# Performance work log

Measured on AMD Instinct MI355X. Metric: run time of the kernel, lower is better.

## Reference

```python
import jax, jax.numpy as jnp
import numpy as np

N_TOKENS = 32768
D_MODEL = 1024


def setup_inputs() -> dict:
    key = jax.random.key(0)
    kx, kr, kw1, kb1, kw2, kb2 = jax.random.split(key, 6)
    scale = 1.0 / np.sqrt(D_MODEL)
    x = jax.random.normal(kx, (N_TOKENS, D_MODEL), dtype=jnp.float32)
    # RandomScatterRouter: each token independently routed to one of 2 experts
    route = jax.random.randint(kr, (N_TOKENS,), 0, 2, dtype=jnp.int32)
    W1 = jax.random.normal(kw1, (D_MODEL, D_MODEL), dtype=jnp.float32) * scale
    b1 = jax.random.normal(kb1, (D_MODEL,), dtype=jnp.float32) * scale
    W2 = jax.random.normal(kw2, (D_MODEL, D_MODEL), dtype=jnp.float32) * scale
    b2 = jax.random.normal(kb2, (D_MODEL,), dtype=jnp.float32) * scale
    return {"x": x, "W1": W1, "b1": b1, "W2": W2, "b2": b2, "route": route}


def reference(x, W1, b1, W2, b2, route):
    # Semantics of scatter -> expert linears -> gather(reverse_indice):
    #   out[i] = x[i] @ W_{route[i]} + b_{route[i]}  (original token order restored)
    # jit-friendly form: mask-partition tokens to each expert (m0 + m1 == 1),
    # run the two expert GEMMs on the disjoint partitions, sum to recombine.
    m0 = (route == 0).astype(x.dtype)[:, None]  # [N, 1]
    m1 = 1.0 - m0
    y0 = (x * m0) @ W1 + b1 * m0  # expert-1 output on its tokens, zeros elsewhere
    y1 = (x * m1) @ W2 + b2 * m1  # expert-2 output on its tokens, zeros elsewhere
    return y0 + y1
```

## Files before the change

### kernel.cpp

```cpp
#include <hip/hip_runtime.h>

#define NT 32768
#define DM 1024
#define NTOT (NT + 128)
#define NKT (DM / 64)

typedef __bf16 bf16x8 __attribute__((ext_vector_type(8)));
typedef float f32x4 __attribute__((ext_vector_type(4)));

#define GLD16(g, l)                                                            \
  __builtin_amdgcn_global_load_lds(                                            \
      (const __attribute__((address_space(1))) void*)(g),                      \
      (__attribute__((address_space(3))) void*)(l), 16, 0, 0)

__device__ __forceinline__ unsigned short f2bf(float f) {
  unsigned u = __float_as_uint(f);
  u += 0x7fffu + ((u >> 16) & 1u);
  return (unsigned short)(u >> 16);
}

__global__ void wt_k(const float* __restrict__ W1, const float* __restrict__ W2,
                     unsigned short* __restrict__ Wt) {
  const float* __restrict__ W = blockIdx.z ? W2 : W1;
  unsigned short* __restrict__ dst = Wt + (size_t)blockIdx.z * DM * DM;
  __shared__ float tile[32][33];
  int tx = threadIdx.x, ty = threadIdx.y;
  int n0 = blockIdx.x * 32, k0 = blockIdx.y * 32;
#pragma unroll
  for (int i = 0; i < 32; i += 8)
    tile[ty + i][tx] = W[(size_t)(k0 + ty + i) * DM + n0 + tx];
  __syncthreads();
#pragma unroll
  for (int i = 0; i < 32; i += 8)
    dst[(size_t)(n0 + ty + i) * DM + k0 + tx] = f2bf(tile[tx][ty + i]);
}

__global__ __launch_bounds__(64) void route_k(const int* __restrict__ route,
                                              int* __restrict__ idx,
                                              int* __restrict__ counters) {
  const int lane = threadIdx.x;
  const int token = blockIdx.x * 64 + lane;
  int r = route[token];
  unsigned long long m0 = __ballot(r == 0);
  unsigned long long lt = (1ULL << lane) - 1ULL;
  int rank0 = __popcll(m0 & lt);
  int rank1 = lane - rank0;
  int cnt0 = __popcll(m0);
  int base0 = 0, base1 = 0;
  if (lane == 0) {
    base0 = atomicAdd(&counters[0], cnt0);
    base1 = atomicAdd(&counters[1], 64 - cnt0);
  }
  base0 = __shfl(base0, 0, 64);
  base1 = __shfl(base1, 0, 64);
  int slot = (r == 0) ? (base0 + rank0) : (NTOT - 1 - (base1 + rank1));
  idx[slot] = token;
}

__global__ __launch_bounds__(256, 3) void gemm_k(
    const float* __restrict__ x,
    const unsigned short* __restrict__ Wt,
    const float* __restrict__ b1, const float* __restrict__ b2,
    const int* __restrict__ idx, const int* __restrict__ counters,
    float* __restrict__ out) {
  __shared__ unsigned short As[128 * 64];
  __shared__ unsigned short Bs[2][128 * 64];

  const int t = threadIdx.x;
  const int lane = t & 63, wave = t >> 6;

  const int lin = blockIdx.y * 8 + blockIdx.x;
  const int L = (lin & 7) * 257 + (lin >> 3);
  const int row0 = (L >> 3) * 128;
  const int col0 = (L & 7) * 128;

  const int n0 = counters[0];
  const int expert = (row0 < n0) ? 0 : 1;
  const unsigned short* Wte = Wt + (size_t)expert * DM * DM;
  const float* bias = expert ? b2 : b1;

  const int wr = (wave >> 1) * 64;
  const int wc = (wave & 1) * 64;
  const int lr = lane & 15;

  const int rsub = t >> 4;
  const int c16 = t & 15;
  const float* rowp[8];
#pragma unroll
  for (int p = 0; p < 8; ++p) {
    int gr = row0 + p * 16 + rsub;
    int tok = idx[gr];
    if (gr >= n0 && gr < n0 + 128) tok = 0;
    rowp[p] = x + (size_t)tok * DM;
  }

  float4 a[8];
  f32x4 acc[4][4] = {};

#define LOADA(k0)                                                              \
  _Pragma("unroll") for (int p = 0; p < 8; ++p)                                \
      a[p] = *(const float4*)(rowp[p] + (k0) + c16 * 4);

#define WRITEA()                                                               \
  _Pragma("unroll") for (int p = 0; p < 8; ++p) {                              \
    int r = p * 16 + rsub;                                                     \
    int off = (r * 8 + ((c16 >> 1) ^ (r & 7))) * 16 + (c16 & 1) * 8;           \
    union { unsigned short h[4]; ushort4 u4; } pk;                             \
    pk.h[0] = f2bf(a[p].x); pk.h[1] = f2bf(a[p].y);                            \
    pk.h[2] = f2bf(a[p].z); pk.h[3] = f2bf(a[p].w);                            \
    *(ushort4*)((char*)&As[0] + off) = pk.u4;                                  \
  }

#define STAGEB(k0, bufw)                                                       \
  _Pragma("unroll") for (int p = 0; p < 4; ++p) {                              \
    int q = p * 256 + t;                                                       \
    int r = q >> 3;                                                            \
    int c = ((q & 7) ^ (r & 7)) * 8;                                           \
    GLD16(Wte + (size_t)(col0 + r) * DM + (k0) + c, &Bs[bufw][q * 8]);         \
  }

  LOADA(0);
  STAGEB(0, 0);

  for (int kt = 0; kt < NKT; ++kt) {
    const int buf = kt & 1;
    WRITEA();
    __syncthreads();
    if (kt < NKT - 1) {
      LOADA((kt + 1) * 64);
      STAGEB((kt + 1) * 64, buf ^ 1);
    }
#pragma unroll
    for (int s = 0; s < 2; ++s) {
      const int cb = s * 4 + (lane >> 4);
      bf16x8 af[4], bfr[4];
#pragma unroll
      for (int i = 0; i < 4; ++i) {
        int r = wr + i * 16 + lr;
        af[i] = *(const bf16x8*)&As[(r * 8 + (cb ^ (r & 7))) * 8];
      }
#pragma unroll
      for (int j = 0; j < 4; ++j) {
        int r = wc + j * 16 + lr;
        bfr[j] = *(const bf16x8*)&Bs[buf][(r * 8 + (cb ^ (r & 7))) * 8];
      }
#pragma unroll
      for (int i = 0; i < 4; ++i)
#pragma unroll
        for (int j = 0; j < 4; ++j)
          acc[i][j] = __builtin_amdgcn_mfma_f32_16x16x32_bf16(af[i], bfr[j], acc[i][j], 0, 0, 0);
    }
    __syncthreads();
  }

#pragma unroll
  for (int i = 0; i < 4; ++i) {
#pragma unroll
    for (int reg = 0; reg < 4; ++reg) {
      int gr = row0 + wr + i * 16 + (lane >> 4) * 4 + reg;
      if (gr < n0 || gr >= n0 + 128) {
        int dest = idx[gr];
#pragma unroll
        for (int j = 0; j < 4; ++j) {
          int gc = col0 + wc + j * 16 + (lane & 15);
          out[(size_t)dest * DM + gc] = acc[i][j][reg] + bias[gc];
        }
      }
    }
  }
#undef LOADA
#undef WRITEA
#undef STAGEB
}

extern "C" void kernel_launch(void* const* d_in, const int* in_sizes, int n_in,
                              void* d_out, int out_size, void* d_ws, size_t ws_size,
                              hipStream_t stream) {
  const float* x   = (const float*)d_in[0];
  const float* W1  = (const float*)d_in[1];
  const float* b1  = (const float*)d_in[2];
  const float* W2  = (const float*)d_in[3];
  const float* b2  = (const float*)d_in[4];
  const int*   route = (const int*)d_in[5];
  float* out = (float*)d_out;

  char* ws = (char*)d_ws;
  unsigned short* Wt = (unsigned short*)ws;
  size_t off = (size_t)2 * DM * DM * 2;
  int* idx = (int*)(ws + off);
  int* counters = idx + NTOT;

  hipMemsetAsync(counters, 0, 2 * sizeof(int), stream);
  route_k<<<NT / 64, 64, 0, stream>>>(route, idx, counters);
  wt_k<<<dim3(DM / 32, DM / 32, 2), dim3(32, 8), 0, stream>>>(W1, W2, Wt);
  gemm_k<<<dim3(8, NTOT / 128), 256, 0, stream>>>(x, Wt, b1, b2, idx, counters, out);
}
```

Before: 357.0 us.

## Single-block route scan, native bf16 convert, unroll K loop, lighter barrier

```diff
diff --git a/kernel.cpp b/kernel.cpp
--- a/kernel.cpp
+++ b/kernel.cpp
@@ -6,6 +6,7 @@
 #define NKT (DM / 64)
 
 typedef __bf16 bf16x8 __attribute__((ext_vector_type(8)));
+typedef __bf16 bf16x4 __attribute__((ext_vector_type(4)));
 typedef float f32x4 __attribute__((ext_vector_type(4)));
 
 #define GLD16(g, l)                                                            \
@@ -35,26 +36,49 @@
     dst[(size_t)(n0 + ty + i) * DM + k0 + tx] = f2bf(tile[tx][ty + i]);
 }
 
-__global__ __launch_bounds__(64) void route_k(const int* __restrict__ route,
-                                              int* __restrict__ idx,
-                                              int* __restrict__ counters) {
-  const int lane = threadIdx.x;
-  const int token = blockIdx.x * 64 + lane;
-  int r = route[token];
-  unsigned long long m0 = __ballot(r == 0);
-  unsigned long long lt = (1ULL << lane) - 1ULL;
-  int rank0 = __popcll(m0 & lt);
-  int rank1 = lane - rank0;
-  int cnt0 = __popcll(m0);
-  int base0 = 0, base1 = 0;
-  if (lane == 0) {
-    base0 = atomicAdd(&counters[0], cnt0);
-    base1 = atomicAdd(&counters[1], 64 - cnt0);
-  }
-  base0 = __shfl(base0, 0, 64);
-  base1 = __shfl(base1, 0, 64);
-  int slot = (r == 0) ? (base0 + rank0) : (NTOT - 1 - (base1 + rank1));
-  idx[slot] = token;
+__global__ __launch_bounds__(1024) void route_k(const int* __restrict__ route,
+                                                int* __restrict__ idx,
+                                                int* __restrict__ counters) {
+  __shared__ int wsum[16];
+  const int t = threadIdx.x;
+  const int lane = t & 63, wv = t >> 6;
+  const int base = t * 32;
+  const int4* rp = (const int4*)(route + base);
+  unsigned mask = 0;
+#pragma unroll
+  for (int v = 0; v < 8; ++v) {
+    int4 q = rp[v];
+    mask |= (unsigned)(q.x == 0) << (v * 4 + 0);
+    mask |= (unsigned)(q.y == 0) << (v * 4 + 1);
+    mask |= (unsigned)(q.z == 0) << (v * 4 + 2);
+    mask |= (unsigned)(q.w == 0) << (v * 4 + 3);
+  }
+  const int c0 = __popc(mask);
+  int s = c0;
+#pragma unroll
+  for (int d = 1; d < 64; d <<= 1) {
+    int v = __shfl_up(s, (unsigned)d, 64);
+    if (lane >= d) s += v;
+  }
+  if (lane == 63) wsum[wv] = s;
+  __syncthreads();
+  int waveBase = 0, total0 = 0;
+#pragma unroll
+  for (int w = 0; w < 16; ++w) {
+    int v = wsum[w];
+    if (w < wv) waveBase += v;
+    total0 += v;
+  }
+  const int ex0 = waveBase + s - c0;
+  int slot0 = ex0;
+  int slot1 = NTOT - 1 - (base - ex0);
+#pragma unroll
+  for (int i = 0; i < 32; ++i) {
+    int token = base + i;
+    if ((mask >> i) & 1) idx[slot0++] = token;
+    else                 idx[slot1--] = token;
+  }
+  if (t == 0) { counters[0] = total0; counters[1] = NT - total0; }
 }
 
 __global__ __launch_bounds__(256, 3) void gemm_k(
@@ -105,10 +129,10 @@
   _Pragma("unroll") for (int p = 0; p < 8; ++p) {                              \
     int r = p * 16 + rsub;                                                     \
     int off = (r * 8 + ((c16 >> 1) ^ (r & 7))) * 16 + (c16 & 1) * 8;           \
-    union { unsigned short h[4]; ushort4 u4; } pk;                             \
-    pk.h[0] = f2bf(a[p].x); pk.h[1] = f2bf(a[p].y);                            \
-    pk.h[2] = f2bf(a[p].z); pk.h[3] = f2bf(a[p].w);                            \
-    *(ushort4*)((char*)&As[0] + off) = pk.u4;                                  \
+    bf16x4 pk;                                                                 \
+    pk[0] = (__bf16)a[p].x; pk[1] = (__bf16)a[p].y;                            \
+    pk[2] = (__bf16)a[p].z; pk[3] = (__bf16)a[p].w;                            \
+    *(bf16x4*)((char*)&As[0] + off) = pk;                                      \
   }
 
 #define STAGEB(k0, bufw)                                                       \
@@ -122,6 +146,7 @@
   LOADA(0);
   STAGEB(0, 0);
 
+#pragma unroll 2
   for (int kt = 0; kt < NKT; ++kt) {
     const int buf = kt & 1;
     WRITEA();
@@ -150,7 +175,10 @@
         for (int j = 0; j < 4; ++j)
           acc[i][j] = __builtin_amdgcn_mfma_f32_16x16x32_bf16(af[i], bfr[j], acc[i][j], 0, 0, 0);
     }
-    __syncthreads();
+    asm volatile("s_waitcnt lgkmcnt(0)" ::: "memory");
+    __builtin_amdgcn_sched_barrier(0);
+    __builtin_amdgcn_s_barrier();
+    __builtin_amdgcn_sched_barrier(0);
   }
 
 #pragma unroll
@@ -190,8 +218,7 @@
   int* idx = (int*)(ws + off);
   int* counters = idx + NTOT;
 
-  hipMemsetAsync(counters, 0, 2 * sizeof(int), stream);
-  route_k<<<NT / 64, 64, 0, stream>>>(route, idx, counters);
+  route_k<<<1, 1024, 0, stream>>>(route, idx, counters);
   wt_k<<<dim3(DM / 32, DM / 32, 2), dim3(32, 8), 0, stream>>>(W1, W2, Wt);
   gemm_k<<<dim3(8, NTOT / 128), 256, 0, stream>>>(x, Wt, b1, b2, idx, counters, out);
 }
```

After: 395.2 us. 10.7% more time.
